# Optimization experiments

Hardware: AMD Instinct MI355X
Metric: run time of the kernel (lower is better)

## Reference

```python
import jax, jax.numpy as jnp
import numpy as np

D = 1024
H = 16
HD = D // H
FF = 4 * D
EPS = 1e-5


def _ln(x, g, b):
    mu = jnp.mean(x, axis=-1, keepdims=True)
    var = jnp.mean(jnp.square(x - mu), axis=-1, keepdims=True)
    return (x - mu) * jax.lax.rsqrt(var + EPS) * g + b


def setup_inputs() -> dict:
    key = jax.random.key(0)
    ks = jax.random.split(key, 16)
    s = 0.02
    return {
        "x": jax.random.normal(ks[0], (2, 2048, D), dtype=jnp.float32),
        "g1": jnp.ones((D,), jnp.float32),
        "b1": jnp.zeros((D,), jnp.float32),
        "Wqkv": jax.random.normal(ks[1], (D, 3 * D), jnp.float32) * s,
        "bqkv": jnp.zeros((3 * D,), jnp.float32),
        "Wo": jax.random.normal(ks[2], (D, D), jnp.float32) * s,
        "bo": jnp.zeros((D,), jnp.float32),
        "g2": jnp.ones((D,), jnp.float32),
        "b2": jnp.zeros((D,), jnp.float32),
        "W1": jax.random.normal(ks[3], (D, FF), jnp.float32) * s,
        "b1f": jnp.zeros((FF,), jnp.float32),
        "W2": jax.random.normal(ks[4], (FF, D), jnp.float32) * s,
        "b2f": jnp.zeros((D,), jnp.float32),
    }


def reference(x, g1, b1, Wqkv, bqkv, Wo, bo, g2, b2, W1, b1f, W2, b2f):
    b, t, d = x.shape
    residual = x
    h = _ln(x, g1, b1)
    qkv = (h @ Wqkv + bqkv).reshape(b, t, 3, H, HD)
    q, k, v = [jnp.transpose(qkv[:, :, i], (0, 2, 1, 3)) for i in range(3)]  # (b,h,t,hd)
    scale = 1.0 / np.sqrt(HD).astype(np.float32)
    attn = jnp.einsum("bhqd,bhkd->bhqk", q, k) * scale
    # cache_offset = 0 in offline mode: mask = (j < 0) | (j <= i) -> causal
    i = jnp.arange(t)[:, None]
    j = jnp.arange(t)[None, :]
    mask = j <= i
    attn = jnp.where(mask, attn, -jnp.inf)
    attn = jax.nn.softmax(attn, axis=-1)
    out = jnp.einsum("bhqk,bhkd->bhqd", attn, v)
    out = jnp.transpose(out, (0, 2, 1, 3)).reshape(b, t, d)
    x = residual + out @ Wo + bo
    hh = _ln(x, g2, b2)
    ff = jax.nn.gelu(hh @ W1 + b1f, approximate=False) @ W2 + b2f
    return x + ff
```

## Files before the change

### kernel.cpp

```cpp
#include <hip/hip_runtime.h>
#include <math.h>

#define TD 1024
#define NH 16
#define HDIM 64
#define SEQ 2048
#define NB 2
#define NROWS 4096
#define FFD 4096

#define QSCALE 0.18033688011112042f

typedef unsigned short u16;
typedef __attribute__((ext_vector_type(8))) short bf16x8;
typedef __attribute__((ext_vector_type(4))) float f32x4;

__device__ __forceinline__ u16 f2bf(float f) {
    union { float f; unsigned u; } v; v.f = f;
    return (u16)((v.u + 0x7FFFu + ((v.u >> 16) & 1u)) >> 16);
}

__device__ __forceinline__ void async16(void* lds, const void* g) {
    __builtin_amdgcn_global_load_lds(
        (const __attribute__((address_space(1))) unsigned*)g,
        (__attribute__((address_space(3))) unsigned*)lds, 16, 0, 0);
}

__global__ __launch_bounds__(256) void ln_bf16(const float* __restrict__ x,
                                               const float* __restrict__ g,
                                               const float* __restrict__ b,
                                               u16* __restrict__ out)
{
    int row = blockIdx.x;
    const float* xr = x + (size_t)row * TD;
    u16* outr = out + (size_t)row * TD;
    int t = threadIdx.x;
    float v[4];
    float s = 0.f, ss = 0.f;
#pragma unroll
    for (int i = 0; i < 4; i++) {
        v[i] = xr[t + 256 * i];
        s += v[i];
        ss += v[i] * v[i];
    }
#pragma unroll
    for (int o = 32; o > 0; o >>= 1) {
        s  += __shfl_down(s, o);
        ss += __shfl_down(ss, o);
    }
    __shared__ float sm[4], sm2[4];
    int wave = t >> 6, lane = t & 63;
    if (lane == 0) { sm[wave] = s; sm2[wave] = ss; }
    __syncthreads();
    s  = sm[0] + sm[1] + sm[2] + sm[3];
    ss = sm2[0] + sm2[1] + sm2[2] + sm2[3];
    float mu  = s * (1.f / TD);
    float var = ss * (1.f / TD) - mu * mu;
    float rstd = rsqrtf(var + 1e-5f);
#pragma unroll
    for (int i = 0; i < 4; i++) {
        int c = t + 256 * i;
        outr[c] = f2bf((v[i] - mu) * rstd * g[c] + b[c]);
    }
}

__global__ __launch_bounds__(256) void wconv_all(
    const float* __restrict__ Wqkv, const float* __restrict__ Wo,
    const float* __restrict__ W1,   const float* __restrict__ W2,
    u16* __restrict__ wqkvT, u16* __restrict__ woT,
    u16* __restrict__ w1T,   u16* __restrict__ w2T)
{
    int blk = blockIdx.x;
    const float* W; u16* Wt; int K, N, local, nx;
    if (blk < 768)       { W = Wqkv; Wt = wqkvT; K = TD;  N = 3 * TD; local = blk;        nx = 48; }
    else if (blk < 1024) { W = Wo;   Wt = woT;   K = TD;  N = TD;     local = blk - 768;  nx = 16; }
    else if (blk < 2048) { W = W1;   Wt = w1T;   K = TD;  N = FFD;    local = blk - 1024; nx = 64; }
    else                 { W = W2;   Wt = w2T;   K = FFD; N = TD;     local = blk - 2048; nx = 16; }
    int n0 = (local % nx) * 64, k0 = (local / nx) * 64;
    __shared__ u16 tile[64][65];
    int t = threadIdx.x, c = t & 63, rq = t >> 6;
#pragma unroll
    for (int i = 0; i < 16; i++) {
        int r = rq * 16 + i;
        tile[r][c] = f2bf(W[(size_t)(k0 + r) * N + n0 + c]);
    }
    __syncthreads();
#pragma unroll
    for (int i = 0; i < 16; i++) {
        int r = rq * 16 + i;
        Wt[(size_t)(n0 + r) * K + k0 + c] = tile[c][r];
    }
}

#define EPI_QKV 0
#define EPI_F32RES 1
#define EPI_GELU 2

template<int EPI, int TN, int BK>
__global__ __launch_bounds__(256) void gemm_mfma(int M, int N, int K,
    const u16* __restrict__ A, const u16* __restrict__ Bt,
    const float* __restrict__ bias, const float* __restrict__ res,
    float* __restrict__ Cf, u16* __restrict__ Cb,
    u16* __restrict__ qb, u16* __restrict__ kb, u16* __restrict__ vb)
{
    constexpr int WN  = TN / 2;
    constexpr int NJ  = WN / 16;
    constexpr int KH  = BK / 32;
    constexpr int CPR = BK / 8;
    constexpr int ACH = (128 * CPR) / 256;
    constexpr int BCH = (TN  * CPR) / 256;
    constexpr int ASZ = 128 * BK * 2;
    constexpr int BSZ = TN  * BK * 2;
    __shared__ __align__(16) char smem[2 * (ASZ + BSZ)];

    int t = threadIdx.x;
    int lane = t & 63, w = t >> 6;
    int wm = w >> 1, wn = w & 1;
    int lr = lane & 15, lq = lane >> 4;
    int gx = gridDim.x;
    int lin = blockIdx.x + gx * blockIdx.y;
    int li = lin >> 3;
    int qy = li / gx;
    int ty = (lin & 7) * (gridDim.y >> 3) + qy;
    int tx = li - qy * gx;
    int m0 = ty * 128, n0 = tx * TN;
    int swc = (lq ^ ((lr >> 1) & 3)) * 16;

    const u16* ap[ACH];
    const u16* bp[BCH];
#pragma unroll
    for (int i = 0; i < ACH; i++) {
        int c = t + 256 * i, r = c / CPR, ww = c % CPR;
        int g = (ww & ~3) | ((ww & 3) ^ ((r >> 1) & 3));
        ap[i] = A + (size_t)(m0 + r) * K + g * 8;
    }
#pragma unroll
    for (int i = 0; i < BCH; i++) {
        int c = t + 256 * i, r = c / CPR, ww = c % CPR;
        int g = (ww & ~3) | ((ww & 3) ^ ((r >> 1) & 3));
        bp[i] = Bt + (size_t)(n0 + r) * K + g * 8;
    }

    f32x4 acc[4][NJ];
#pragma unroll
    for (int i = 0; i < 4; i++)
#pragma unroll
        for (int j = 0; j < NJ; j++) acc[i][j] = (f32x4){0.f, 0.f, 0.f, 0.f};

#pragma unroll
    for (int i = 0; i < ACH; i++)
        async16(smem + (t + 256 * i) * 16, ap[i]);
#pragma unroll
    for (int i = 0; i < BCH; i++)
        async16(smem + 2 * ASZ + (t + 256 * i) * 16, bp[i]);

    int nk = K / BK;
    for (int kt = 0; kt < nk; kt++) {
        int cur = kt & 1;
        __syncthreads();
        if (kt + 1 < nk) {
            char* An = smem + (1 - cur) * ASZ;
            char* Bn = smem + 2 * ASZ + (1 - cur) * BSZ;
#pragma unroll
            for (int i = 0; i < ACH; i++) {
                ap[i] += BK;
                async16(An + (t + 256 * i) * 16, ap[i]);
            }
#pragma unroll
            for (int i = 0; i < BCH; i++) {
                bp[i] += BK;
                async16(Bn + (t + 256 * i) * 16, bp[i]);
            }
        }
        const char* Ac = smem + cur * ASZ;
        const char* Bc = smem + 2 * ASZ + cur * BSZ;
#pragma unroll
        for (int h = 0; h < KH; h++) {
            bf16x8 af[4], bfr[NJ];
#pragma unroll
            for (int i = 0; i < 4; i++)
                af[i] = *(const bf16x8*)(Ac + (wm * 64 + i * 16 + lr) * (2 * BK) + h * 64 + swc);
#pragma unroll
            for (int j = 0; j < NJ; j++)
                bfr[j] = *(const bf16x8*)(Bc + (wn * WN + j * 16 + lr) * (2 * BK) + h * 64 + swc);
#pragma unroll
            for (int i = 0; i < 4; i++)
#pragma unroll
                for (int j = 0; j < NJ; j++)
                    acc[i][j] = __builtin_amdgcn_mfma_f32_16x16x32_bf16(af[i], bfr[j], acc[i][j], 0, 0, 0);
        }
    }

#pragma unroll
    for (int i = 0; i < 4; i++) {
        int rowb = m0 + wm * 64 + i * 16 + lq * 4;
#pragma unroll
        for (int j = 0; j < NJ; j++) {
            int col = n0 + wn * WN + j * 16 + lr;
            float bs = bias[col];
            float vals[4];
#pragma unroll
            for (int r = 0; r < 4; r++) vals[r] = acc[i][j][r] + bs;
            if (EPI == EPI_F32RES) {
#pragma unroll
                for (int r = 0; r < 4; r++) {
                    int rr = rowb + r;
                    Cf[(size_t)rr * N + col] = vals[r] + res[(size_t)rr * N + col];
                }
            } else if (EPI == EPI_GELU) {
#pragma unroll
                for (int r = 0; r < 4; r++) {
                    float v = vals[r];
                    v = 0.5f * v * (1.f + erff(v * 0.70710678118654752f));
                    Cb[(size_t)(rowb + r) * N + col] = f2bf(v);
                }
            } else {
                int comp = col >> 10, cw = col & 1023;
                int h = cw >> 6, d = cw & 63;
                int bb0 = rowb >> 11, ts = rowb & 2047;
                int bh = bb0 * NH + h;
                if (comp == 0) {
#pragma unroll
                    for (int r = 0; r < 4; r++)
                        qb[((size_t)bh * SEQ + ts + r) * HDIM + d] = f2bf(vals[r] * QSCALE);
                } else if (comp == 1) {
#pragma unroll
                    for (int r = 0; r < 4; r++)
                        kb[((size_t)bh * SEQ + ts + r) * HDIM + d] = f2bf(vals[r]);
                } else {
                    ushort4 pk;
                    pk.x = f2bf(vals[0]); pk.y = f2bf(vals[1]);
                    pk.z = f2bf(vals[2]); pk.w = f2bf(vals[3]);
                    *(ushort4*)&vb[((size_t)bh * HDIM + d) * SEQ + ts] = pk;
                }
            }
        }
    }
}

__global__ __launch_bounds__(256, 4) void attn_mfma(const u16* __restrict__ qb,
                                                    const u16* __restrict__ kb,
                                                    const u16* __restrict__ vb,
                                                    u16* __restrict__ ctx)
{
    __shared__ __align__(16) char smem[40960];
    char* QP = smem;
    int bh = blockIdx.y, bb = bh >> 4, h = bh & 15;
    int t = threadIdx.x, lane = t & 63, w = t >> 6;
    int lr = lane & 15, lq = lane >> 4;
    int sw = (lr & 7) * 16;
    int cA = (lq * 16) ^ sw;
    int cB = (64 | (lq * 16)) ^ sw;
    int c0 = t,        r0 = c0 >> 3, g0 = (c0 & 7) ^ (r0 & 7);
    int c1 = t + 256,  r1 = c1 >> 3, g1 = (c1 & 7) ^ (r1 & 7);
    size_t off0  = (size_t)r0 * 128  + g0 * 16;
    size_t off1  = (size_t)r1 * 128  + g1 * 16;
    size_t voff0 = (size_t)r0 * 4096 + g0 * 16;
    size_t voff1 = (size_t)r1 * 4096 + g1 * 16;

    const char* qg_base = (const char*)qb + (size_t)bh * SEQ * 128;
    const char* kg_base = (const char*)kb + (size_t)bh * SEQ * 128;
    const char* vg_base = (const char*)vb + (size_t)bh * 64 * 4096;

    for (int pass = 0; pass < 2; ++pass) {
        int qt = pass ? blockIdx.x : (31 - blockIdx.x);
        if (pass) __syncthreads();
        const char* qg = qg_base + (size_t)qt * 8192;
        async16(QP + c0 * 16, qg + off0);
        async16(QP + c1 * 16, qg + off1);
        async16(smem + 8192 + c0 * 16, kg_base + off0);
        async16(smem + 8192 + c1 * 16, kg_base + off1);
        async16(smem + 24576 + c0 * 16, vg_base + voff0);
        async16(smem + 24576 + c1 * 16, vg_base + voff1);

        float mold = -INFINITY, lsum = 0.f;
        f32x4 o[4];
#pragma unroll
        for (int dj = 0; dj < 4; dj++) o[dj] = (f32x4){0.f, 0.f, 0.f, 0.f};
        bf16x8 bq0, bq1;

        for (int kt = 0; kt <= qt; ++kt) {
            int cur = kt & 1;
            __syncthreads();
            if (kt < qt) {
                const char* kgn = kg_base + (size_t)(kt + 1) * 8192;
                const char* vgn = vg_base + (size_t)(kt + 1) * 128;
                char* Kn = smem + 8192  + (1 - cur) * 8192;
                char* Vn = smem + 24576 + (1 - cur) * 8192;
                async16(Kn + c0 * 16, kgn + off0);
                async16(Kn + c1 * 16, kgn + off1);
                async16(Vn + c0 * 16, vgn + voff0);
                async16(Vn + c1 * 16, vgn + voff1);
            }
            if (kt == 0) {
                const char* qr = QP + (w * 16 + lr) * 128;
                bq0 = *(const bf16x8*)(qr + cA);
                bq1 = *(const bf16x8*)(qr + cB);
            }
            const char* Kc = smem + 8192  + cur * 8192;
            const char* Vc = smem + 24576 + cur * 8192;

            float sv[4][4];
            bool diag = (kt == qt);
#pragma unroll
            for (int j = 0; j < 4; ++j) {
                const char* kr = Kc + (j * 16 + lr) * 128;
                bf16x8 ak0 = *(const bf16x8*)(kr + cA);
                bf16x8 ak1 = *(const bf16x8*)(kr + cB);
                f32x4 z = (f32x4){0.f, 0.f, 0.f, 0.f};
                z = __builtin_amdgcn_mfma_f32_16x16x32_bf16(ak0, bq0, z, 0, 0, 0);
                z = __builtin_amdgcn_mfma_f32_16x16x32_bf16(ak1, bq1, z, 0, 0, 0);
#pragma unroll
                for (int r = 0; r < 4; r++) {
                    float xv = z[r];
                    if (diag && (j * 16 + lq * 4 + r > w * 16 + lr)) xv = -INFINITY;
                    sv[j][r] = xv;
                }
            }
            float mx = sv[0][0];
#pragma unroll
            for (int j = 0; j < 4; j++)
#pragma unroll
                for (int r = 0; r < 4; r++) mx = fmaxf(mx, sv[j][r]);
            mx = fmaxf(mx, __shfl_xor(mx, 16));
            mx = fmaxf(mx, __shfl_xor(mx, 32));
            float mnew = fmaxf(mold, mx);
            float alpha = exp2f(mold - mnew);
            float rs = 0.f;
            unsigned pk[4][2];
#pragma unroll
            for (int j = 0; j < 4; j++)
#pragma unroll
                for (int hh = 0; hh < 2; hh++) {
                    float p0 = exp2f(sv[j][2 * hh]     - mnew);
                    float p1 = exp2f(sv[j][2 * hh + 1] - mnew);
                    rs += p0 + p1;
                    pk[j][hh] = (unsigned)f2bf(p0) | ((unsigned)f2bf(p1) << 16);
                }
            rs += __shfl_xor(rs, 16);
            rs += __shfl_xor(rs, 32);
            lsum = lsum * alpha + rs;
            mold = mnew;
#pragma unroll
            for (int dj = 0; dj < 4; dj++)
#pragma unroll
                for (int r = 0; r < 4; r++) o[dj][r] *= alpha;

            {
                char* pw = QP + (w * 16 + lr) * 128 + (lq & 1) * 8;
#pragma unroll
                for (int j = 0; j < 4; j++) {
                    int pos = ((j * 2 + (lq >> 1)) * 16) ^ sw;
                    uint2 u; u.x = pk[j][0]; u.y = pk[j][1];
                    *(uint2*)(pw + pos) = u;
                }
            }
            asm volatile("s_waitcnt lgkmcnt(0)" ::: "memory");
            const char* pr = QP + (w * 16 + lr) * 128;
            bf16x8 bp0 = *(const bf16x8*)(pr + cA);
            bf16x8 bp1 = *(const bf16x8*)(pr + cB);
#pragma unroll
            for (int dj = 0; dj < 4; ++dj) {
                const char* vr = Vc + (dj * 16 + lr) * 128;
                bf16x8 av0 = *(const bf16x8*)(vr + cA);
                bf16x8 av1 = *(const bf16x8*)(vr + cB);
                o[dj] = __builtin_amdgcn_mfma_f32_16x16x32_bf16(av0, bp0, o[dj], 0, 0, 0);
                o[dj] = __builtin_amdgcn_mfma_f32_16x16x32_bf16(av1, bp1, o[dj], 0, 0, 0);
            }
        }

        float inv = 1.f / lsum;
        int tok = qt * 64 + w * 16 + lr;
        u16* cp = ctx + ((size_t)(bb * SEQ) + tok) * TD + h * HDIM + lq * 4;
#pragma unroll
        for (int dj = 0; dj < 4; dj++) {
            ushort4 s4;
            s4.x = f2bf(o[dj][0] * inv); s4.y = f2bf(o[dj][1] * inv);
            s4.z = f2bf(o[dj][2] * inv); s4.w = f2bf(o[dj][3] * inv);
            *(ushort4*)(cp + dj * 16) = s4;
        }
    }
}

extern "C" void kernel_launch(void* const* d_in, const int* in_sizes, int n_in,
                              void* d_out, int out_size, void* d_ws, size_t ws_size,
                              hipStream_t stream)
{
    const float* x    = (const float*)d_in[0];
    const float* g1   = (const float*)d_in[1];
    const float* b1   = (const float*)d_in[2];
    const float* Wqkv = (const float*)d_in[3];
    const float* bqkv = (const float*)d_in[4];
    const float* Wo   = (const float*)d_in[5];
    const float* bo   = (const float*)d_in[6];
    const float* g2   = (const float*)d_in[7];
    const float* b2   = (const float*)d_in[8];
    const float* W1   = (const float*)d_in[9];
    const float* b1f  = (const float*)d_in[10];
    const float* W2   = (const float*)d_in[11];
    const float* b2f  = (const float*)d_in[12];
    float* out = (float*)d_out;

    char* ws = (char*)d_ws;
    const size_t MB = 1ull << 20;
    u16* wqkvT = (u16*)(ws + 0 * MB);
    u16* woT   = (u16*)(ws + 6 * MB);
    u16* w1T   = (u16*)(ws + 8 * MB);
    u16* w2T   = (u16*)(ws + 16 * MB);
    u16* qbuf  = (u16*)(ws + 24 * MB);
    u16* kbuf  = (u16*)(ws + 32 * MB);
    u16* vbuf  = (u16*)(ws + 40 * MB);
    u16* hbuf  = (u16*)(ws + 48 * MB);
    u16* ctx   = (u16*)(ws + 56 * MB);
    float* x2  = (float*)(ws + 64 * MB);
    u16* ff1   = (u16*)(ws + 80 * MB);

    wconv_all<<<3072, 256, 0, stream>>>(Wqkv, Wo, W1, W2, wqkvT, woT, w1T, w2T);

    ln_bf16<<<NROWS, 256, 0, stream>>>(x, g1, b1, hbuf);
    gemm_mfma<EPI_QKV, 128, 64><<<dim3(3 * TD / 128, NROWS / 128), 256, 0, stream>>>(
        NROWS, 3 * TD, TD, hbuf, wqkvT, bqkv, nullptr, nullptr, nullptr, qbuf, kbuf, vbuf);
    attn_mfma<<<dim3(16, NB * NH), 256, 0, stream>>>(qbuf, kbuf, vbuf, ctx);
    gemm_mfma<EPI_F32RES, 64, 64><<<dim3(TD / 64, NROWS / 128), 256, 0, stream>>>(
        NROWS, TD, TD, ctx, woT, bo, x, x2, nullptr, nullptr, nullptr, nullptr);
    ln_bf16<<<NROWS, 256, 0, stream>>>(x2, g2, b2, hbuf);
    gemm_mfma<EPI_GELU, 128, 64><<<dim3(FFD / 128, NROWS / 128), 256, 0, stream>>>(
        NROWS, FFD, TD, hbuf, w1T, b1f, nullptr, nullptr, ff1, nullptr, nullptr, nullptr);
    gemm_mfma<EPI_F32RES, 64, 64><<<dim3(TD / 64, NROWS / 128), 256, 0, stream>>>(
        NROWS, TD, FFD, ff1, w2T, b2f, x2, out, nullptr, nullptr, nullptr, nullptr);
}
```

Baseline: 334.4 us.

## Fuse first layernorm into weight-conversion launch, remap attention blocks across XCDs, truncate P to bf16

The first layernorm now runs as extra blocks of the weight-conversion kernel, which removes one kernel launch and lets the two independent jobs overlap. The attention grid index is remapped so that each XCD handles a set of heads, aiming to improve L2 locality for the K/V reads. The round-to-nearest bf16 packing of softmax probabilities is replaced by a single byte-permute truncation, which saves ALU work in the inner loop but rounds the probabilities slightly less accurately.

```diff
diff --git a/kernel.cpp b/kernel.cpp
--- a/kernel.cpp
+++ b/kernel.cpp
@@ -64,13 +64,49 @@
     }
 }
 
-__global__ __launch_bounds__(256) void wconv_all(
+__global__ __launch_bounds__(256) void prep_kernel(
     const float* __restrict__ Wqkv, const float* __restrict__ Wo,
     const float* __restrict__ W1,   const float* __restrict__ W2,
     u16* __restrict__ wqkvT, u16* __restrict__ woT,
-    u16* __restrict__ w1T,   u16* __restrict__ w2T)
+    u16* __restrict__ w1T,   u16* __restrict__ w2T,
+    const float* __restrict__ x, const float* __restrict__ g1,
+    const float* __restrict__ b1, u16* __restrict__ hbuf)
 {
     int blk = blockIdx.x;
+    int t = threadIdx.x;
+    if (blk >= 3072) {
+        int row = blk - 3072;
+        const float* xr = x + (size_t)row * TD;
+        u16* outr = hbuf + (size_t)row * TD;
+        float v[4];
+        float s = 0.f, ss = 0.f;
+#pragma unroll
+        for (int i = 0; i < 4; i++) {
+            v[i] = xr[t + 256 * i];
+            s += v[i];
+            ss += v[i] * v[i];
+        }
+#pragma unroll
+        for (int o = 32; o > 0; o >>= 1) {
+            s  += __shfl_down(s, o);
+            ss += __shfl_down(ss, o);
+        }
+        __shared__ float sm[4], sm2[4];
+        int wave = t >> 6, lane = t & 63;
+        if (lane == 0) { sm[wave] = s; sm2[wave] = ss; }
+        __syncthreads();
+        s  = sm[0] + sm[1] + sm[2] + sm[3];
+        ss = sm2[0] + sm2[1] + sm2[2] + sm2[3];
+        float mu  = s * (1.f / TD);
+        float var = ss * (1.f / TD) - mu * mu;
+        float rstd = rsqrtf(var + 1e-5f);
+#pragma unroll
+        for (int i = 0; i < 4; i++) {
+            int c = t + 256 * i;
+            outr[c] = f2bf((v[i] - mu) * rstd * g1[c] + b1[c]);
+        }
+        return;
+    }
     const float* W; u16* Wt; int K, N, local, nx;
     if (blk < 768)       { W = Wqkv; Wt = wqkvT; K = TD;  N = 3 * TD; local = blk;        nx = 48; }
     else if (blk < 1024) { W = Wo;   Wt = woT;   K = TD;  N = TD;     local = blk - 768;  nx = 16; }
@@ -78,7 +114,7 @@
     else                 { W = W2;   Wt = w2T;   K = FFD; N = TD;     local = blk - 2048; nx = 16; }
     int n0 = (local % nx) * 64, k0 = (local / nx) * 64;
     __shared__ u16 tile[64][65];
-    int t = threadIdx.x, c = t & 63, rq = t >> 6;
+    int c = t & 63, rq = t >> 6;
 #pragma unroll
     for (int i = 0; i < 16; i++) {
         int r = rq * 16 + i;
@@ -245,7 +281,11 @@
 {
     __shared__ __align__(16) char smem[40960];
     char* QP = smem;
-    int bh = blockIdx.y, bb = bh >> 4, h = bh & 15;
+    int lin = blockIdx.x + 16 * blockIdx.y;
+    int xcd = lin & 7, idx = lin >> 3;
+    int bh = xcd + 8 * (idx & 3);
+    int bx = idx >> 2;
+    int bb = bh >> 4, h = bh & 15;
     int t = threadIdx.x, lane = t & 63, w = t >> 6;
     int lr = lane & 15, lq = lane >> 4;
     int sw = (lr & 7) * 16;
@@ -263,7 +303,7 @@
     const char* vg_base = (const char*)vb + (size_t)bh * 64 * 4096;
 
     for (int pass = 0; pass < 2; ++pass) {
-        int qt = pass ? blockIdx.x : (31 - blockIdx.x);
+        int qt = pass ? bx : (31 - bx);
         if (pass) __syncthreads();
         const char* qg = qg_base + (size_t)qt * 8192;
         async16(QP + c0 * 16, qg + off0);
@@ -335,7 +375,9 @@
                     float p0 = exp2f(sv[j][2 * hh]     - mnew);
                     float p1 = exp2f(sv[j][2 * hh + 1] - mnew);
                     rs += p0 + p1;
-                    pk[j][hh] = (unsigned)f2bf(p0) | ((unsigned)f2bf(p1) << 16);
+                    union { float f; unsigned u; } a0, a1;
+                    a0.f = p0; a1.f = p1;
+                    pk[j][hh] = __builtin_amdgcn_perm(a1.u, a0.u, 0x07060302u);
                 }
             rs += __shfl_xor(rs, 16);
             rs += __shfl_xor(rs, 32);
@@ -415,9 +457,9 @@
     float* x2  = (float*)(ws + 64 * MB);
     u16* ff1   = (u16*)(ws + 80 * MB);
 
-    wconv_all<<<3072, 256, 0, stream>>>(Wqkv, Wo, W1, W2, wqkvT, woT, w1T, w2T);
-
-    ln_bf16<<<NROWS, 256, 0, stream>>>(x, g1, b1, hbuf);
+    prep_kernel<<<3072 + NROWS, 256, 0, stream>>>(
+        Wqkv, Wo, W1, W2, wqkvT, woT, w1T, w2T, x, g1, b1, hbuf);
+
     gemm_mfma<EPI_QKV, 128, 64><<<dim3(3 * TD / 128, NROWS / 128), 256, 0, stream>>>(
         NROWS, 3 * TD, TD, hbuf, wqkvT, bqkv, nullptr, nullptr, nullptr, qbuf, kbuf, vbuf);
     attn_mfma<<<dim3(16, NB * NH), 256, 0, stream>>>(qbuf, kbuf, vbuf, ctx);
```

New measurement: 328.0 us. No clear change (-1.9%).
